# Optimization experiments

Measured on AMD Instinct MI355X. Metric: run time of the kernel, lower is better.

## Reference

```python
import jax, jax.numpy as jnp
import numpy as np

MIN_VALUE = float(np.finfo(np.float32).min)


def setup_inputs() -> dict:
    key = jax.random.key(0)
    kq, kk, ki = jax.random.split(key, 3)
    B, T, C = 8, 2048, 512
    q = jax.random.normal(kq, (B, 1, T, C), dtype=jnp.float32)
    k = jax.random.normal(kk, (B, 1, T, C), dtype=jnp.float32)
    ilens = jax.random.randint(ki, (B,), T // 2, T + 1).astype(jnp.int32)
    ilens = ilens.at[0].set(T)  # ensure max(ilens) == T as in the torch forward
    return {"q": q, "k": k, "ilens": ilens}


def _fb(energy_t):
    # energy_t: (B, 1, T). Batched cumulative-product kernel target (mode='batch', offset=1).
    x = energy_t[:, 0]                       # (B, T)
    B, T = x.shape
    tri = jnp.triu(jnp.ones((T, T), x.dtype), 1)          # m_f
    # xs[b, i, j] = x[b, i]; tril keeps j <= i, upper strict triangle set to 1
    X = jnp.tril(jnp.broadcast_to(x[:, :, None], (B, T, T))) + tri
    xf = jnp.cumprod(X, axis=-2)                           # cumprod over rows
    # offset = 1: shift rows down by one, prepend ones row, subtract m_f
    xf = jnp.concatenate([jnp.ones((B, 1, T), x.dtype), xf[:, :-1]], axis=1) - tri
    return xf[:, None]                                     # (B, 1, T, T)


def reference(q, k, ilens):
    B, H, T, C = q.shape
    # make_pad_mask: True at padded positions
    pad = jnp.arange(T)[None, :] >= ilens[:, None]                     # (B, T)
    valid = (~pad).astype(q.dtype)
    mask = (1.0 - valid[:, :, None] * valid[:, None, :]).astype(bool)  # (B, T, T)
    mask = mask[:, None]                                               # (B, 1, T, T)
    eye = jnp.eye(T, dtype=bool)[None, None]

    # attn(q, k, mask, mask_diag=True): score[t, s] = k[t] . q[s] / sqrt(C)
    score = jnp.einsum('bhtc,bhsc->bhts', k, q) / jnp.sqrt(jnp.asarray(C, q.dtype))
    score = jnp.where(eye | mask, MIN_VALUE, score)
    kernel = jax.nn.softmax(score, axis=-1)
    kernel = jnp.where(eye | mask, 0.0, kernel)
    c = jnp.einsum('bhts,bhsc->bhtc', kernel, q)

    # self-similarity of keys
    kernel_kk = jnp.einsum('bhtc,bhsc->bhts', k, k)

    # energy chain (no-grad in the original) -> fb cumprod kernel target
    kq = jax.lax.stop_gradient(kernel)
    diag1 = jnp.diagonal(kq, offset=1, axis1=-2, axis2=-1)             # (B, 1, T-1)
    energy_t = jnp.concatenate([jnp.ones_like(diag1[..., :1]), 1.0 - diag1], axis=-1)
    kernel_target = _fb(energy_t)                                      # (B, 1, T, T)

    return c, kernel, score, kernel_kk, kernel_target
```

## Files before the change

kernel.cpp:

```cpp
#include <hip/hip_runtime.h>

constexpr int B = 8;
constexpr int T = 2048;
constexpr int C = 512;
constexpr float MASK_VALUE = -3.3895313892515355e+38f;
constexpr float MIN_VALUE  = -3.4028234663852886e+38f;

#define BKG 16
#define LDSS 68

__global__ __launch_bounds__(256) void gemm_nt_kernel(
    const float* __restrict__ A, const float* __restrict__ Bm,
    float* __restrict__ D, const int* __restrict__ ilens, int mode)
{
    int b   = blockIdx.z;
    int tm0 = blockIdx.y * 64;
    int tn0 = blockIdx.x * 64;
    const float* Ab = A + (size_t)b * T * C;
    const float* Bb = Bm + (size_t)b * T * C;
    float* Db = D + (size_t)b * T * T;

    __shared__ float As[BKG][LDSS];
    __shared__ float Bs[BKG][LDSS];

    int tid = threadIdx.x;
    int tx = tid & 15;
    int ty = tid >> 4;
    int lr = tid >> 2;
    int lk = (tid & 3) << 2;

    float acc[4][4];
#pragma unroll
    for (int i = 0; i < 4; ++i)
#pragma unroll
        for (int j = 0; j < 4; ++j) acc[i][j] = 0.f;

    for (int k0 = 0; k0 < C; k0 += BKG) {
        float4 av = *reinterpret_cast<const float4*>(Ab + (size_t)(tm0 + lr) * C + k0 + lk);
        float4 bv = *reinterpret_cast<const float4*>(Bb + (size_t)(tn0 + lr) * C + k0 + lk);
        __syncthreads();
        As[lk + 0][lr] = av.x; As[lk + 1][lr] = av.y; As[lk + 2][lr] = av.z; As[lk + 3][lr] = av.w;
        Bs[lk + 0][lr] = bv.x; Bs[lk + 1][lr] = bv.y; Bs[lk + 2][lr] = bv.z; Bs[lk + 3][lr] = bv.w;
        __syncthreads();
#pragma unroll
        for (int kk = 0; kk < BKG; ++kk) {
            float4 a  = *reinterpret_cast<const float4*>(&As[kk][ty * 4]);
            float4 bq = *reinterpret_cast<const float4*>(&Bs[kk][tx * 4]);
            float aa[4] = {a.x, a.y, a.z, a.w};
            float bb[4] = {bq.x, bq.y, bq.z, bq.w};
#pragma unroll
            for (int i = 0; i < 4; ++i)
#pragma unroll
                for (int j = 0; j < 4; ++j)
                    acc[i][j] = fmaf(aa[i], bb[j], acc[i][j]);
        }
    }

    int ilen = (mode == 1) ? ilens[b] : 0;
    float sc = sqrtf((float)C);
#pragma unroll
    for (int i = 0; i < 4; ++i) {
        int t  = tm0 + ty * 4 + i;
        int sb = tn0 + tx * 4;
        float vv[4];
#pragma unroll
        for (int j = 0; j < 4; ++j) {
            float v = acc[i][j];
            if (mode == 1) {
                v = v / sc;
                int s = sb + j;
                if (t == s || t >= ilen || s >= ilen) v = MASK_VALUE;
            }
            vv[j] = v;
        }
        float4 o = {vv[0], vv[1], vv[2], vv[3]};
        *reinterpret_cast<float4*>(Db + (size_t)t * T + sb) = o;
    }
}

__global__ __launch_bounds__(256) void gemm_nn_kernel(
    const float* __restrict__ A, const float* __restrict__ Bm, float* __restrict__ D)
{
    int b   = blockIdx.z;
    int tm0 = blockIdx.y * 64;
    int tn0 = blockIdx.x * 64;
    const float* Ab = A + (size_t)b * T * T;
    const float* Bb = Bm + (size_t)b * T * C;
    float* Db = D + (size_t)b * T * C;

    __shared__ float As[BKG][LDSS];
    __shared__ float Bs[BKG][LDSS];

    int tid = threadIdx.x;
    int tx = tid & 15;
    int ty = tid >> 4;
    int lr = tid >> 2;
    int lk = (tid & 3) << 2;
    int bkr = tid >> 4;
    int bcb = (tid & 15) << 2;

    float acc[4][4];
#pragma unroll
    for (int i = 0; i < 4; ++i)
#pragma unroll
        for (int j = 0; j < 4; ++j) acc[i][j] = 0.f;

    for (int k0 = 0; k0 < T; k0 += BKG) {
        float4 av = *reinterpret_cast<const float4*>(Ab + (size_t)(tm0 + lr) * T + k0 + lk);
        float4 bv = *reinterpret_cast<const float4*>(Bb + (size_t)(k0 + bkr) * C + tn0 + bcb);
        __syncthreads();
        As[lk + 0][lr] = av.x; As[lk + 1][lr] = av.y; As[lk + 2][lr] = av.z; As[lk + 3][lr] = av.w;
        *reinterpret_cast<float4*>(&Bs[bkr][bcb]) = bv;
        __syncthreads();
#pragma unroll
        for (int kk = 0; kk < BKG; ++kk) {
            float4 a  = *reinterpret_cast<const float4*>(&As[kk][ty * 4]);
            float4 bq = *reinterpret_cast<const float4*>(&Bs[kk][tx * 4]);
            float aa[4] = {a.x, a.y, a.z, a.w};
            float bb[4] = {bq.x, bq.y, bq.z, bq.w};
#pragma unroll
            for (int i = 0; i < 4; ++i)
#pragma unroll
                for (int j = 0; j < 4; ++j)
                    acc[i][j] = fmaf(aa[i], bb[j], acc[i][j]);
        }
    }

#pragma unroll
    for (int i = 0; i < 4; ++i) {
        int t  = tm0 + ty * 4 + i;
        int cb = tn0 + tx * 4;
        float4 o = {acc[i][0], acc[i][1], acc[i][2], acc[i][3]};
        *reinterpret_cast<float4*>(Db + (size_t)t * C + cb) = o;
    }
}

__global__ __launch_bounds__(256) void softmax_kernel(
    const float* __restrict__ score, float* __restrict__ kern,
    const int* __restrict__ ilens)
{
    int row = blockIdx.x;
    int b = row >> 11;
    int t = row & (T - 1);
    const float* src = score + (size_t)row * T;
    float* dst = kern + (size_t)row * T;
    int tid = threadIdx.x;
    int ilen = ilens[b];

    if (t >= ilen) {
        for (int s = tid; s < T; s += 256) dst[s] = 0.f;
        return;
    }

    float vals[8];
    float m = MIN_VALUE;
#pragma unroll
    for (int i = 0; i < 8; ++i) {
        vals[i] = src[tid + i * 256];
        m = fmaxf(m, vals[i]);
    }
    for (int off = 32; off > 0; off >>= 1) m = fmaxf(m, __shfl_down(m, off, 64));
    __shared__ float redm[4];
    __shared__ float reds[4];
    int wid = tid >> 6, lane = tid & 63;
    if (lane == 0) redm[wid] = m;
    __syncthreads();
    m = fmaxf(fmaxf(redm[0], redm[1]), fmaxf(redm[2], redm[3]));

    float ex[8];
    float sum = 0.f;
#pragma unroll
    for (int i = 0; i < 8; ++i) {
        ex[i] = expf(vals[i] - m);
        sum += ex[i];
    }
    for (int off = 32; off > 0; off >>= 1) sum += __shfl_down(sum, off, 64);
    if (lane == 0) reds[wid] = sum;
    __syncthreads();
    sum = (reds[0] + reds[1]) + (reds[2] + reds[3]);
    float inv = 1.f / sum;
#pragma unroll
    for (int i = 0; i < 8; ++i) dst[tid + i * 256] = ex[i] * inv;
}

__global__ __launch_bounds__(256) void target_kernel(
    const float* __restrict__ kern, float* __restrict__ out)
{
    int b = blockIdx.y;
    int tid = threadIdx.x;
    int j = blockIdx.x * 256 + tid;

    __shared__ float xs[T];
    const float* kb = kern + (size_t)b * T * T;
    for (int i = tid; i < T; i += 256)
        xs[i] = (i == 0) ? 1.f : 1.f - kb[(size_t)(i - 1) * T + i];
    __syncthreads();

    float* ob = out + (size_t)b * T * T;
    float p = 0.f;
    for (int i = 0; i < T; ++i) {
        float v;
        if (i < j)       v = 0.f;
        else if (i == j) { p = 1.f; v = 1.f; }
        else             { p *= xs[i - 1]; v = p; }
        ob[(size_t)i * T + j] = v;
    }
}

extern "C" void kernel_launch(void* const* d_in, const int* in_sizes, int n_in,
                              void* d_out, int out_size, void* d_ws, size_t ws_size,
                              hipStream_t stream)
{
    const float* q     = (const float*)d_in[0];
    const float* k     = (const float*)d_in[1];
    const int*   ilens = (const int*)d_in[2];

    float* out = (float*)d_out;
    const size_t cN = (size_t)B * T * C;
    const size_t sN = (size_t)B * T * T;
    float* c_out     = out;
    float* kern_out  = out + cN;
    float* score_out = out + cN + sN;
    float* kk_out    = out + cN + 2 * sN;
    float* tgt_out   = out + cN + 3 * sN;

    dim3 g1(T / 64, T / 64, B);
    hipLaunchKernelGGL(gemm_nt_kernel, g1, dim3(256), 0, stream, k, q, score_out, ilens, 1);
    hipLaunchKernelGGL(gemm_nt_kernel, g1, dim3(256), 0, stream, k, k, kk_out, ilens, 0);
    hipLaunchKernelGGL(softmax_kernel, dim3(B * T), dim3(256), 0, stream, score_out, kern_out, ilens);
    dim3 g2(C / 64, T / 64, B);
    hipLaunchKernelGGL(gemm_nn_kernel, g2, dim3(256), 0, stream, kern_out, q, c_out);
    hipLaunchKernelGGL(target_kernel, dim3(T / 256, B), dim3(256), 0, stream, kern_out, tgt_out);
}
```

Before: 2.051 ms.

## Use 128x128 register-blocked GEMM tiles with register prefetch of next K slice

Both GEMM kernels move from 64x64 tiles with 4x4 per-thread outputs to 128x128 tiles with 8x8 per-thread outputs. This raises arithmetic intensity per shared-memory load, and the next K slice is loaded into registers while the current one is computed. The division by sqrt(C) becomes a multiply by a constant, and softmax is launched right after the score GEMM instead of after the kk GEMM. The cost is higher register pressure (64 accumulators) and fewer blocks for the small c GEMM (4x16x8 = 512 blocks), which may lower occupancy.

```diff
diff --git a/kernel.cpp b/kernel.cpp
--- a/kernel.cpp
+++ b/kernel.cpp
@@ -6,75 +6,99 @@
 constexpr float MASK_VALUE = -3.3895313892515355e+38f;
 constexpr float MIN_VALUE  = -3.4028234663852886e+38f;
 
-#define BKG 16
-#define LDSS 68
+#define BK 16
+#define LDP 132
 
 __global__ __launch_bounds__(256) void gemm_nt_kernel(
     const float* __restrict__ A, const float* __restrict__ Bm,
     float* __restrict__ D, const int* __restrict__ ilens, int mode)
 {
     int b   = blockIdx.z;
-    int tm0 = blockIdx.y * 64;
-    int tn0 = blockIdx.x * 64;
+    int tm0 = blockIdx.y * 128;
+    int tn0 = blockIdx.x * 128;
     const float* Ab = A + (size_t)b * T * C;
     const float* Bb = Bm + (size_t)b * T * C;
     float* Db = D + (size_t)b * T * T;
 
-    __shared__ float As[BKG][LDSS];
-    __shared__ float Bs[BKG][LDSS];
-
-    int tid = threadIdx.x;
-    int tx = tid & 15;
-    int ty = tid >> 4;
-    int lr = tid >> 2;
-    int lk = (tid & 3) << 2;
-
-    float acc[4][4];
-#pragma unroll
-    for (int i = 0; i < 4; ++i)
-#pragma unroll
-        for (int j = 0; j < 4; ++j) acc[i][j] = 0.f;
-
-    for (int k0 = 0; k0 < C; k0 += BKG) {
-        float4 av = *reinterpret_cast<const float4*>(Ab + (size_t)(tm0 + lr) * C + k0 + lk);
-        float4 bv = *reinterpret_cast<const float4*>(Bb + (size_t)(tn0 + lr) * C + k0 + lk);
-        __syncthreads();
-        As[lk + 0][lr] = av.x; As[lk + 1][lr] = av.y; As[lk + 2][lr] = av.z; As[lk + 3][lr] = av.w;
-        Bs[lk + 0][lr] = bv.x; Bs[lk + 1][lr] = bv.y; Bs[lk + 2][lr] = bv.z; Bs[lk + 3][lr] = bv.w;
-        __syncthreads();
-#pragma unroll
-        for (int kk = 0; kk < BKG; ++kk) {
-            float4 a  = *reinterpret_cast<const float4*>(&As[kk][ty * 4]);
-            float4 bq = *reinterpret_cast<const float4*>(&Bs[kk][tx * 4]);
-            float aa[4] = {a.x, a.y, a.z, a.w};
-            float bb[4] = {bq.x, bq.y, bq.z, bq.w};
-#pragma unroll
-            for (int i = 0; i < 4; ++i)
-#pragma unroll
-                for (int j = 0; j < 4; ++j)
+    __shared__ float As[BK][LDP];
+    __shared__ float Bs[BK][LDP];
+
+    int tid  = threadIdx.x;
+    int tx   = tid & 15;
+    int ty   = tid >> 4;
+    int lrow = tid >> 2;
+    int lk4  = (tid & 3) << 2;
+
+    const float* Apt = Ab + (size_t)(tm0 + lrow) * C + lk4;
+    const float* Bpt = Bb + (size_t)(tn0 + lrow) * C + lk4;
+
+    float acc[8][8];
+#pragma unroll
+    for (int i = 0; i < 8; ++i)
+#pragma unroll
+        for (int j = 0; j < 8; ++j) acc[i][j] = 0.f;
+
+    float4 a0 = *reinterpret_cast<const float4*>(Apt);
+    float4 a1 = *reinterpret_cast<const float4*>(Apt + (size_t)64 * C);
+    float4 b0 = *reinterpret_cast<const float4*>(Bpt);
+    float4 b1 = *reinterpret_cast<const float4*>(Bpt + (size_t)64 * C);
+
+    for (int k0 = 0; k0 < C; k0 += BK) {
+        __syncthreads();
+        As[lk4 + 0][lrow] = a0.x; As[lk4 + 1][lrow] = a0.y;
+        As[lk4 + 2][lrow] = a0.z; As[lk4 + 3][lrow] = a0.w;
+        As[lk4 + 0][64 + lrow] = a1.x; As[lk4 + 1][64 + lrow] = a1.y;
+        As[lk4 + 2][64 + lrow] = a1.z; As[lk4 + 3][64 + lrow] = a1.w;
+        Bs[lk4 + 0][lrow] = b0.x; Bs[lk4 + 1][lrow] = b0.y;
+        Bs[lk4 + 2][lrow] = b0.z; Bs[lk4 + 3][lrow] = b0.w;
+        Bs[lk4 + 0][64 + lrow] = b1.x; Bs[lk4 + 1][64 + lrow] = b1.y;
+        Bs[lk4 + 2][64 + lrow] = b1.z; Bs[lk4 + 3][64 + lrow] = b1.w;
+        __syncthreads();
+
+        if (k0 + BK < C) {
+            a0 = *reinterpret_cast<const float4*>(Apt + k0 + BK);
+            a1 = *reinterpret_cast<const float4*>(Apt + (size_t)64 * C + k0 + BK);
+            b0 = *reinterpret_cast<const float4*>(Bpt + k0 + BK);
+            b1 = *reinterpret_cast<const float4*>(Bpt + (size_t)64 * C + k0 + BK);
+        }
+
+#pragma unroll
+        for (int kk = 0; kk < BK; ++kk) {
+            float4 av0 = *reinterpret_cast<const float4*>(&As[kk][ty * 8]);
+            float4 av1 = *reinterpret_cast<const float4*>(&As[kk][ty * 8 + 4]);
+            float4 bv0 = *reinterpret_cast<const float4*>(&Bs[kk][tx * 8]);
+            float4 bv1 = *reinterpret_cast<const float4*>(&Bs[kk][tx * 8 + 4]);
+            float aa[8] = {av0.x, av0.y, av0.z, av0.w, av1.x, av1.y, av1.z, av1.w};
+            float bb[8] = {bv0.x, bv0.y, bv0.z, bv0.w, bv1.x, bv1.y, bv1.z, bv1.w};
+#pragma unroll
+            for (int i = 0; i < 8; ++i)
+#pragma unroll
+                for (int j = 0; j < 8; ++j)
                     acc[i][j] = fmaf(aa[i], bb[j], acc[i][j]);
         }
     }
 
     int ilen = (mode == 1) ? ilens[b] : 0;
-    float sc = sqrtf((float)C);
-#pragma unroll
-    for (int i = 0; i < 4; ++i) {
-        int t  = tm0 + ty * 4 + i;
-        int sb = tn0 + tx * 4;
-        float vv[4];
-#pragma unroll
-        for (int j = 0; j < 4; ++j) {
+    const float inv_sc = 0.044194173824159216f;
+#pragma unroll
+    for (int i = 0; i < 8; ++i) {
+        int t  = tm0 + ty * 8 + i;
+        int sb = tn0 + tx * 8;
+        float vv[8];
+#pragma unroll
+        for (int j = 0; j < 8; ++j) {
             float v = acc[i][j];
             if (mode == 1) {
-                v = v / sc;
+                v = v * inv_sc;
                 int s = sb + j;
                 if (t == s || t >= ilen || s >= ilen) v = MASK_VALUE;
             }
             vv[j] = v;
         }
-        float4 o = {vv[0], vv[1], vv[2], vv[3]};
-        *reinterpret_cast<float4*>(Db + (size_t)t * T + sb) = o;
+        float4 o0 = {vv[0], vv[1], vv[2], vv[3]};
+        float4 o1 = {vv[4], vv[5], vv[6], vv[7]};
+        *reinterpret_cast<float4*>(Db + (size_t)t * T + sb)     = o0;
+        *reinterpret_cast<float4*>(Db + (size_t)t * T + sb + 4) = o1;
     }
 }
 
@@ -82,56 +106,78 @@
     const float* __restrict__ A, const float* __restrict__ Bm, float* __restrict__ D)
 {
     int b   = blockIdx.z;
-    int tm0 = blockIdx.y * 64;
-    int tn0 = blockIdx.x * 64;
+    int tm0 = blockIdx.y * 128;
+    int tn0 = blockIdx.x * 128;
     const float* Ab = A + (size_t)b * T * T;
     const float* Bb = Bm + (size_t)b * T * C;
     float* Db = D + (size_t)b * T * C;
 
-    __shared__ float As[BKG][LDSS];
-    __shared__ float Bs[BKG][LDSS];
-
-    int tid = threadIdx.x;
-    int tx = tid & 15;
-    int ty = tid >> 4;
-    int lr = tid >> 2;
-    int lk = (tid & 3) << 2;
-    int bkr = tid >> 4;
-    int bcb = (tid & 15) << 2;
-
-    float acc[4][4];
-#pragma unroll
-    for (int i = 0; i < 4; ++i)
-#pragma unroll
-        for (int j = 0; j < 4; ++j) acc[i][j] = 0.f;
-
-    for (int k0 = 0; k0 < T; k0 += BKG) {
-        float4 av = *reinterpret_cast<const float4*>(Ab + (size_t)(tm0 + lr) * T + k0 + lk);
-        float4 bv = *reinterpret_cast<const float4*>(Bb + (size_t)(k0 + bkr) * C + tn0 + bcb);
-        __syncthreads();
-        As[lk + 0][lr] = av.x; As[lk + 1][lr] = av.y; As[lk + 2][lr] = av.z; As[lk + 3][lr] = av.w;
-        *reinterpret_cast<float4*>(&Bs[bkr][bcb]) = bv;
-        __syncthreads();
-#pragma unroll
-        for (int kk = 0; kk < BKG; ++kk) {
-            float4 a  = *reinterpret_cast<const float4*>(&As[kk][ty * 4]);
-            float4 bq = *reinterpret_cast<const float4*>(&Bs[kk][tx * 4]);
-            float aa[4] = {a.x, a.y, a.z, a.w};
-            float bb[4] = {bq.x, bq.y, bq.z, bq.w};
-#pragma unroll
-            for (int i = 0; i < 4; ++i)
-#pragma unroll
-                for (int j = 0; j < 4; ++j)
+    __shared__ float As[BK][LDP];
+    __shared__ float Bs[BK][LDP];
+
+    int tid  = threadIdx.x;
+    int tx   = tid & 15;
+    int ty   = tid >> 4;
+    int lrow = tid >> 2;
+    int lk4  = (tid & 3) << 2;
+    int bkr  = tid >> 4;
+    int bc0  = (tid & 15) << 2;
+
+    const float* Apt = Ab + (size_t)(tm0 + lrow) * T + lk4;
+    const float* Bpt = Bb + (size_t)bkr * C + tn0 + bc0;
+
+    float acc[8][8];
+#pragma unroll
+    for (int i = 0; i < 8; ++i)
+#pragma unroll
+        for (int j = 0; j < 8; ++j) acc[i][j] = 0.f;
+
+    float4 a0 = *reinterpret_cast<const float4*>(Apt);
+    float4 a1 = *reinterpret_cast<const float4*>(Apt + (size_t)64 * T);
+    float4 b0 = *reinterpret_cast<const float4*>(Bpt);
+    float4 b1 = *reinterpret_cast<const float4*>(Bpt + 64);
+
+    for (int k0 = 0; k0 < T; k0 += BK) {
+        __syncthreads();
+        As[lk4 + 0][lrow] = a0.x; As[lk4 + 1][lrow] = a0.y;
+        As[lk4 + 2][lrow] = a0.z; As[lk4 + 3][lrow] = a0.w;
+        As[lk4 + 0][64 + lrow] = a1.x; As[lk4 + 1][64 + lrow] = a1.y;
+        As[lk4 + 2][64 + lrow] = a1.z; As[lk4 + 3][64 + lrow] = a1.w;
+        *reinterpret_cast<float4*>(&Bs[bkr][bc0])      = b0;
+        *reinterpret_cast<float4*>(&Bs[bkr][64 + bc0]) = b1;
+        __syncthreads();
+
+        if (k0 + BK < T) {
+            a0 = *reinterpret_cast<const float4*>(Apt + k0 + BK);
+            a1 = *reinterpret_cast<const float4*>(Apt + (size_t)64 * T + k0 + BK);
+            b0 = *reinterpret_cast<const float4*>(Bpt + (size_t)(k0 + BK) * C);
+            b1 = *reinterpret_cast<const float4*>(Bpt + (size_t)(k0 + BK) * C + 64);
+        }
+
+#pragma unroll
+        for (int kk = 0; kk < BK; ++kk) {
+            float4 av0 = *reinterpret_cast<const float4*>(&As[kk][ty * 8]);
+            float4 av1 = *reinterpret_cast<const float4*>(&As[kk][ty * 8 + 4]);
+            float4 bv0 = *reinterpret_cast<const float4*>(&Bs[kk][tx * 8]);
+            float4 bv1 = *reinterpret_cast<const float4*>(&Bs[kk][tx * 8 + 4]);
+            float aa[8] = {av0.x, av0.y, av0.z, av0.w, av1.x, av1.y, av1.z, av1.w};
+            float bb[8] = {bv0.x, bv0.y, bv0.z, bv0.w, bv1.x, bv1.y, bv1.z, bv1.w};
+#pragma unroll
+            for (int i = 0; i < 8; ++i)
+#pragma unroll
+                for (int j = 0; j < 8; ++j)
                     acc[i][j] = fmaf(aa[i], bb[j], acc[i][j]);
         }
     }
 
 #pragma unroll
-    for (int i = 0; i < 4; ++i) {
-        int t  = tm0 + ty * 4 + i;
-        int cb = tn0 + tx * 4;
-        float4 o = {acc[i][0], acc[i][1], acc[i][2], acc[i][3]};
-        *reinterpret_cast<float4*>(Db + (size_t)t * C + cb) = o;
+    for (int i = 0; i < 8; ++i) {
+        int t  = tm0 + ty * 8 + i;
+        int cb = tn0 + tx * 8;
+        float4 o0 = {acc[i][0], acc[i][1], acc[i][2], acc[i][3]};
+        float4 o1 = {acc[i][4], acc[i][5], acc[i][6], acc[i][7]};
+        *reinterpret_cast<float4*>(Db + (size_t)t * C + cb)     = o0;
+        *reinterpret_cast<float4*>(Db + (size_t)t * C + cb + 4) = o1;
     }
 }
 
@@ -224,11 +270,11 @@
     float* kk_out    = out + cN + 2 * sN;
     float* tgt_out   = out + cN + 3 * sN;
 
-    dim3 g1(T / 64, T / 64, B);
+    dim3 g1(T / 128, T / 128, B);
     hipLaunchKernelGGL(gemm_nt_kernel, g1, dim3(256), 0, stream, k, q, score_out, ilens, 1);
+    hipLaunchKernelGGL(softmax_kernel, dim3(B * T), dim3(256), 0, stream, score_out, kern_out, ilens);
     hipLaunchKernelGGL(gemm_nt_kernel, g1, dim3(256), 0, stream, k, k, kk_out, ilens, 0);
-    hipLaunchKernelGGL(softmax_kernel, dim3(B * T), dim3(256), 0, stream, score_out, kern_out, ilens);
-    dim3 g2(C / 64, T / 64, B);
+    dim3 g2(C / 128, T / 128, B);
     hipLaunchKernelGGL(gemm_nn_kernel, g2, dim3(256), 0, stream, kern_out, q, c_out);
     hipLaunchKernelGGL(target_kernel, dim3(T / 256, B), dim3(256), 0, stream, kern_out, tgt_out);
 }
```

Result: no change. 2.077 ms (+1.3%).
